# Kernel tuning notes

Measured on AMD Instinct MI355X. Metric: run time of the kernel, lower is better.

## Reference

```python
import jax, jax.numpy as jnp
import numpy as np

B, N, DIM, NL, E = 8, 4096, 128, 3, 524288
NN = B * N


def setup_inputs() -> dict:
    key = jax.random.key(0)
    kx, ke, kw = jax.random.split(key, 3)
    x = jax.random.normal(kx, (B, N, DIM), dtype=jnp.float32)
    batch_edge_index = jax.random.randint(ke, (2, E), 0, NN, dtype=jnp.int32)
    wks = jax.random.split(kw, NL)
    Ws = jnp.stack([jax.random.normal(k, (DIM, DIM), dtype=jnp.float32) / np.sqrt(DIM)
                    for k in wks])  # [NL, DIM, DIM]
    bs = jnp.zeros((NL, DIM), dtype=jnp.float32)
    return {"x": x, "batch_edge_index": batch_edge_index, "Ws": Ws, "bs": bs}


def _gcn_layer(x, W, b, row, col, deg_inv_sqrt, n):
    # PyG GCNConv: h = x @ W; symmetric normalization over edges+self-loops;
    # scatter-add messages at targets (col); add bias.
    h = x @ W  # [n, DIM]
    norm = deg_inv_sqrt[row] * deg_inv_sqrt[col]  # [E+n]
    msg = h[row] * norm[:, None]  # gather at sources, scale
    return jax.ops.segment_sum(msg, col, num_segments=n) + b


def reference(x, batch_edge_index, Ws, bs):
    nb, npts, d = x.shape
    n = nb * npts
    h = x.reshape(n, d)
    # add self-loops once (same edge structure for all layers)
    loops = jnp.arange(n, dtype=batch_edge_index.dtype)
    row = jnp.concatenate([batch_edge_index[0], loops])
    col = jnp.concatenate([batch_edge_index[1], loops])
    deg = jax.ops.segment_sum(jnp.ones_like(col, dtype=h.dtype), col, num_segments=n)
    deg_inv_sqrt = jnp.where(deg > 0, jax.lax.rsqrt(jnp.maximum(deg, 1e-12)), 0.0)
    for i in range(NL):
        out = _gcn_layer(h, Ws[i], bs[i], row, col, deg_inv_sqrt, n)
        h = jax.nn.relu(h + out)  # residual + relu (dropout = identity in eval)
    return h.reshape(nb, npts, d)
```

## Files before the change

kernel.cpp:

```cpp
#include <hip/hip_runtime.h>


typedef __attribute__((ext_vector_type(8))) short short8;
typedef __attribute__((ext_vector_type(4))) float f32x4;
typedef __attribute__((ext_vector_type(2))) float f32x2;

__device__ inline ushort f2bf(float f) {
    union { float f; unsigned u; } v; v.f = f;
    unsigned u = v.u;
    return (ushort)((u + 0x7fffu + ((u >> 16) & 1u)) >> 16);
}
__device__ inline float2 bf2f(unsigned u) {
    union { unsigned i; float f; } a, b;
    a.i = u << 16;
    b.i = u & 0xffff0000u;
    return make_float2(a.f, b.f);
}

__global__ void k_deg(const int* __restrict__ col, int* __restrict__ deg, int E) {
    int i = blockIdx.x * blockDim.x + threadIdx.x;
    if (i < E) atomicAdd(&deg[col[i]], 1);
}

__global__ __launch_bounds__(256) void k_scan1(const int* __restrict__ deg,
                                               int* __restrict__ offs,
                                               int* __restrict__ bsum, int n) {
    __shared__ int sm[256];
    int t = threadIdx.x, i = blockIdx.x * 256 + t;
    int v = (i < n) ? deg[i] : 0;
    sm[t] = v;
    __syncthreads();
    for (int off = 1; off < 256; off <<= 1) {
        int u = (t >= off) ? sm[t - off] : 0;
        __syncthreads();
        sm[t] += u;
        __syncthreads();
    }
    if (i < n) offs[i] = sm[t] - v;
    if (t == 255) bsum[blockIdx.x] = sm[255];
}

__global__ __launch_bounds__(128) void k_scan2(int* __restrict__ bsum, int nb) {
    __shared__ int sm[128];
    int t = threadIdx.x;
    int v = (t < nb) ? bsum[t] : 0;
    sm[t] = v;
    __syncthreads();
    for (int off = 1; off < 128; off <<= 1) {
        int u = (t >= off) ? sm[t - off] : 0;
        __syncthreads();
        sm[t] += u;
        __syncthreads();
    }
    if (t < nb) bsum[t] = sm[t] - v;
}

__global__ __launch_bounds__(256) void k_scan3(int* __restrict__ offs,
                                               const int* __restrict__ bsum,
                                               const int* __restrict__ deg,
                                               int* __restrict__ cnt,
                                               float* __restrict__ dis,
                                               int n, int E) {
    int i = blockIdx.x * 256 + threadIdx.x;
    if (i < n) {
        int o = offs[i] + bsum[blockIdx.x];
        offs[i] = o;
        cnt[i] = o;
        dis[i] = rsqrtf((float)(deg[i] + 1));
    }
    if (i == 0) offs[n] = E;
}

__global__ void k_csr(const int* __restrict__ row, const int* __restrict__ col,
                      int* __restrict__ cnt, ushort* __restrict__ csru, int E) {
    int i = blockIdx.x * blockDim.x + threadIdx.x;
    if (i < E) {
        int c = col[i];
        int p = atomicAdd(&cnt[c], 1);
        csru[p] = (ushort)row[i];
    }
}

__global__ void k_cvt(const float* __restrict__ x, unsigned* __restrict__ hb,
                      unsigned* __restrict__ g, int n) {
    int i = blockIdx.x * blockDim.x + threadIdx.x;
    if (i < n * 64) {
        float2 v = ((const float2*)x)[i];
        hb[i] = ((unsigned)f2bf(v.y) << 16) | f2bf(v.x);
    }
    if (i < 64) g[(size_t)n * 64 + i] = 0;
}

__global__ __launch_bounds__(256) void k_gemm(const unsigned* __restrict__ hb,
                                              const float* __restrict__ W,
                                              const float* __restrict__ dis,
                                              ushort* __restrict__ g, int n) {
    __shared__ unsigned Wl[128][64];
    int tid = threadIdx.x;
    {
        int nn = tid & 127, hf = tid >> 7;
        for (int q = 0; q < 32; ++q) {
            int k2 = hf * 32 + q;
            float lo = W[(size_t)(2 * k2) * 128 + nn];
            float hi = W[(size_t)(2 * k2 + 1) * 128 + nn];
            Wl[nn][k2 ^ ((nn & 7) << 2)] = ((unsigned)f2bf(hi) << 16) | f2bf(lo);
        }
    }
    __syncthreads();

    int w = tid >> 6, l = tid & 63;
    int rb = blockIdx.x * 64 + w * 16;
    int c = l & 15, q = l >> 4;

    const short8* arow = (const short8*)(hb + (size_t)(rb + c) * 64);
    short8 a0 = arow[q], a1 = arow[4 + q], a2 = arow[8 + q], a3 = arow[12 + q];

    f32x4 acc[8] = {};
#pragma unroll
    for (int nf = 0; nf < 8; ++nf) {
        const unsigned* wr = &Wl[nf * 16 + c][0];
        int s = (c & 7) << 2;
        int b = q * 4;
        short8 b0 = *(const short8*)(wr + ((b +  0) ^ s));
        short8 b1 = *(const short8*)(wr + ((b + 16) ^ s));
        short8 b2 = *(const short8*)(wr + ((b + 32) ^ s));
        short8 b3 = *(const short8*)(wr + ((b + 48) ^ s));
        acc[nf] = __builtin_amdgcn_mfma_f32_16x16x32_bf16(a0, b0, acc[nf], 0, 0, 0);
        acc[nf] = __builtin_amdgcn_mfma_f32_16x16x32_bf16(a1, b1, acc[nf], 0, 0, 0);
        acc[nf] = __builtin_amdgcn_mfma_f32_16x16x32_bf16(a2, b2, acc[nf], 0, 0, 0);
        acc[nf] = __builtin_amdgcn_mfma_f32_16x16x32_bf16(a3, b3, acc[nf], 0, 0, 0);
    }

    float d0 = dis[rb + q * 4 + 0], d1 = dis[rb + q * 4 + 1];
    float d2 = dis[rb + q * 4 + 2], d3 = dis[rb + q * 4 + 3];
#pragma unroll
    for (int nf = 0; nf < 8; ++nf) {
        int gc = nf * 16 + c;
        g[(size_t)(rb + q * 4 + 0) * 128 + gc] = f2bf(acc[nf][0] * d0);
        g[(size_t)(rb + q * 4 + 1) * 128 + gc] = f2bf(acc[nf][1] * d1);
        g[(size_t)(rb + q * 4 + 2) * 128 + gc] = f2bf(acc[nf][2] * d2);
        g[(size_t)(rb + q * 4 + 3) * 128 + gc] = f2bf(acc[nf][3] * d3);
    }
}

__global__ __launch_bounds__(256) void k_gather(const unsigned* __restrict__ g,
                                                unsigned* __restrict__ hb,
                                                const float* __restrict__ dis,
                                                const float2* __restrict__ bias2,
                                                const int* __restrict__ offs,
                                                const ushort* __restrict__ csru,
                                                float* __restrict__ outp,
                                                int n, int last) {
    int wid = threadIdx.x >> 6, lane = threadIdx.x & 63;
    int node = blockIdx.x * 4 + wid;
    if (node >= n) return;
    size_t nb = (size_t)node * 64 + lane;
    float2 acc = bf2f(g[nb]);
    int s = offs[node];
    int deg = offs[node + 1] - s;
    for (int j0 = 0; j0 < deg; j0 += 64) {
        int rem = deg - j0;
        int m = rem < 64 ? rem : 64;
        int idx = (lane < m) ? (int)__builtin_nontemporal_load(&csru[s + j0 + lane]) : n;
        int mc = (m + 15) & ~15;
        for (int t = 0; t < mc; t += 16) {
            unsigned v[16];
#pragma unroll
            for (int u = 0; u < 16; ++u)
                v[u] = g[(size_t)__shfl(idx, t + u, 64) * 64 + lane];
            float2 p0, p1;
#define ACC2(A, B, O)  p0 = bf2f(v[A]); p1 = bf2f(v[B]); \
                       O.x = p0.x + p1.x; O.y = p0.y + p1.y;
            float2 s0, s1, s2, s3, s4, s5, s6, s7;
            ACC2(0, 1, s0)  ACC2(2, 3, s1)  ACC2(4, 5, s2)  ACC2(6, 7, s3)
            ACC2(8, 9, s4)  ACC2(10, 11, s5) ACC2(12, 13, s6) ACC2(14, 15, s7)
#undef ACC2
            s0.x += s1.x; s2.x += s3.x; s4.x += s5.x; s6.x += s7.x;
            s0.y += s1.y; s2.y += s3.y; s4.y += s5.y; s6.y += s7.y;
            acc.x += (s0.x + s2.x) + (s4.x + s6.x);
            acc.y += (s0.y + s2.y) + (s4.y + s6.y);
        }
    }
    float d = dis[node];
    float2 bv = bias2[lane];
    float2 hv = bf2f(hb[nb]);
    float ox = fmaxf(hv.x + acc.x * d + bv.x, 0.f);
    float oy = fmaxf(hv.y + acc.y * d + bv.y, 0.f);
    if (last) {
        f32x2 o = { ox, oy };
        __builtin_nontemporal_store(o, (f32x2*)&outp[(size_t)node * 128 + lane * 2]);
    } else {
        hb[nb] = ((unsigned)f2bf(oy) << 16) | f2bf(ox);
    }
}

static inline size_t al256(size_t x) { return (x + 255) & ~(size_t)255; }

extern "C" void kernel_launch(void* const* d_in, const int* in_sizes, int n_in,
                              void* d_out, int out_size, void* d_ws, size_t ws_size,
                              hipStream_t stream) {
    const float* x  = (const float*)d_in[0];
    const int*   ei = (const int*)d_in[1];
    const float* Ws = (const float*)d_in[2];
    const float* bs = (const float*)d_in[3];
    int n  = in_sizes[0] / 128;
    int E  = in_sizes[1] / 2;
    int NL = in_sizes[2] / (128 * 128);
    const int* rowp = ei;
    const int* colp = ei + E;

    char* ws = (char*)d_ws;
    size_t plane = al256((size_t)(n + 1) * 256);
    unsigned* g  = (unsigned*)ws;
    unsigned* hb = (unsigned*)(ws + plane);
    char* p = ws + 2 * plane;
    float* dis  = (float*)p;               p += al256((size_t)n * 4);
    int*   deg  = (int*)p;                 p += al256((size_t)n * 4);
    int*   offs = (int*)p;                 p += al256((size_t)(n + 1) * 4);
    int*   cnt  = (int*)p;                 p += al256((size_t)n * 4);
    int*   bsum = (int*)p;                 p += 512;
    ushort* csru = (ushort*)p;

    int nb = (n + 255) / 256;

    (void)hipMemsetAsync(deg, 0, (size_t)n * 4, stream);
    k_deg<<<(E + 255) / 256, 256, 0, stream>>>(colp, deg, E);
    k_scan1<<<nb, 256, 0, stream>>>(deg, offs, bsum, n);
    k_scan2<<<1, 128, 0, stream>>>(bsum, nb);
    k_scan3<<<nb, 256, 0, stream>>>(offs, bsum, deg, cnt, dis, n, E);
    k_csr<<<(E + 255) / 256, 256, 0, stream>>>(rowp, colp, cnt, csru, E);
    k_cvt<<<(n * 64 + 255) / 256, 256, 0, stream>>>(x, hb, g, n);

    for (int l = 0; l < NL; ++l) {
        int last = (l + 1 == NL);
        k_gemm<<<n / 64, 256, 0, stream>>>(hb, Ws + (size_t)l * 128 * 128,
                                           dis, (ushort*)g, n);
        k_gather<<<(n + 3) / 4, 256, 0, stream>>>(g, hb, dis,
                                                  (const float2*)(bs + (size_t)l * 128),
                                                  offs, csru, (float*)d_out, n, last);
    }
}
```

Before: 165.0 us.

## Fuse fp32 input conversion into first GEMM and widen gather to 8-byte half-wave loads

```diff
diff --git a/kernel.cpp b/kernel.cpp
--- a/kernel.cpp
+++ b/kernel.cpp
@@ -3,7 +3,6 @@
 
 typedef __attribute__((ext_vector_type(8))) short short8;
 typedef __attribute__((ext_vector_type(4))) float f32x4;
-typedef __attribute__((ext_vector_type(2))) float f32x2;
 
 __device__ inline ushort f2bf(float f) {
     union { float f; unsigned u; } v; v.f = f;
@@ -15,6 +14,16 @@
     a.i = u << 16;
     b.i = u & 0xffff0000u;
     return make_float2(a.f, b.f);
+}
+__device__ inline f32x4 bf4(uint2 v) {
+    float2 a = bf2f(v.x), b = bf2f(v.y);
+    f32x4 r = { a.x, a.y, b.x, b.y };
+    return r;
+}
+__device__ inline short8 pack8(f32x4 a, f32x4 b) {
+    short8 r = { (short)f2bf(a.x), (short)f2bf(a.y), (short)f2bf(a.z), (short)f2bf(a.w),
+                 (short)f2bf(b.x), (short)f2bf(b.y), (short)f2bf(b.z), (short)f2bf(b.w) };
+    return r;
 }
 
 __global__ void k_deg(const int* __restrict__ col, int* __restrict__ deg, int E) {
@@ -60,6 +69,7 @@
                                                const int* __restrict__ deg,
                                                int* __restrict__ cnt,
                                                float* __restrict__ dis,
+                                               unsigned* __restrict__ g,
                                                int n, int E) {
     int i = blockIdx.x * 256 + threadIdx.x;
     if (i < n) {
@@ -69,6 +79,7 @@
         dis[i] = rsqrtf((float)(deg[i] + 1));
     }
     if (i == 0) offs[n] = E;
+    if (i < 64) g[(size_t)n * 64 + i] = 0;
 }
 
 __global__ void k_csr(const int* __restrict__ row, const int* __restrict__ col,
@@ -81,81 +92,92 @@
     }
 }
 
-__global__ void k_cvt(const float* __restrict__ x, unsigned* __restrict__ hb,
-                      unsigned* __restrict__ g, int n) {
-    int i = blockIdx.x * blockDim.x + threadIdx.x;
-    if (i < n * 64) {
-        float2 v = ((const float2*)x)[i];
-        hb[i] = ((unsigned)f2bf(v.y) << 16) | f2bf(v.x);
-    }
-    if (i < 64) g[(size_t)n * 64 + i] = 0;
-}
+#define GEMM_BODY(A0, A1, A2, A3)                                               \
+    f32x4 acc[8] = {};                                                          \
+    _Pragma("unroll")                                                           \
+    for (int nf = 0; nf < 8; ++nf) {                                            \
+        const unsigned* wr = &Wl[nf * 16 + c][0];                               \
+        int sx = (c & 7) << 2;                                                  \
+        int b = q * 4;                                                          \
+        short8 b0 = *(const short8*)(wr + ((b +  0) ^ sx));                     \
+        short8 b1 = *(const short8*)(wr + ((b + 16) ^ sx));                     \
+        short8 b2 = *(const short8*)(wr + ((b + 32) ^ sx));                     \
+        short8 b3 = *(const short8*)(wr + ((b + 48) ^ sx));                     \
+        acc[nf] = __builtin_amdgcn_mfma_f32_16x16x32_bf16(A0, b0, acc[nf], 0, 0, 0); \
+        acc[nf] = __builtin_amdgcn_mfma_f32_16x16x32_bf16(A1, b1, acc[nf], 0, 0, 0); \
+        acc[nf] = __builtin_amdgcn_mfma_f32_16x16x32_bf16(A2, b2, acc[nf], 0, 0, 0); \
+        acc[nf] = __builtin_amdgcn_mfma_f32_16x16x32_bf16(A3, b3, acc[nf], 0, 0, 0); \
+    }                                                                           \
+    float d0 = dis[rb + q * 4 + 0], d1 = dis[rb + q * 4 + 1];                   \
+    float d2 = dis[rb + q * 4 + 2], d3 = dis[rb + q * 4 + 3];                   \
+    _Pragma("unroll")                                                           \
+    for (int nf = 0; nf < 8; ++nf) {                                            \
+        int gc = nf * 16 + c;                                                   \
+        g[(size_t)(rb + q * 4 + 0) * 128 + gc] = f2bf(acc[nf][0] * d0);         \
+        g[(size_t)(rb + q * 4 + 1) * 128 + gc] = f2bf(acc[nf][1] * d1);         \
+        g[(size_t)(rb + q * 4 + 2) * 128 + gc] = f2bf(acc[nf][2] * d2);         \
+        g[(size_t)(rb + q * 4 + 3) * 128 + gc] = f2bf(acc[nf][3] * d3);         \
+    }
+
+#define W_STAGE                                                                  \
+    __shared__ unsigned Wl[128][64];                                             \
+    int tid = threadIdx.x;                                                       \
+    {                                                                            \
+        int nn = tid & 127, hf = tid >> 7;                                       \
+        for (int qq = 0; qq < 32; ++qq) {                                        \
+            int k2 = hf * 32 + qq;                                               \
+            float lo = W[(size_t)(2 * k2) * 128 + nn];                           \
+            float hi = W[(size_t)(2 * k2 + 1) * 128 + nn];                       \
+            Wl[nn][k2 ^ ((nn & 7) << 2)] = ((unsigned)f2bf(hi) << 16) | f2bf(lo);\
+        }                                                                        \
+    }                                                                            \
+    __syncthreads();                                                             \
+    int w = tid >> 6, l = tid & 63;                                              \
+    int rb = blockIdx.x * 64 + w * 16;                                           \
+    int c = l & 15, q = l >> 4;
 
 __global__ __launch_bounds__(256) void k_gemm(const unsigned* __restrict__ hb,
                                               const float* __restrict__ W,
                                               const float* __restrict__ dis,
                                               ushort* __restrict__ g, int n) {
-    __shared__ unsigned Wl[128][64];
-    int tid = threadIdx.x;
-    {
-        int nn = tid & 127, hf = tid >> 7;
-        for (int q = 0; q < 32; ++q) {
-            int k2 = hf * 32 + q;
-            float lo = W[(size_t)(2 * k2) * 128 + nn];
-            float hi = W[(size_t)(2 * k2 + 1) * 128 + nn];
-            Wl[nn][k2 ^ ((nn & 7) << 2)] = ((unsigned)f2bf(hi) << 16) | f2bf(lo);
-        }
-    }
-    __syncthreads();
-
-    int w = tid >> 6, l = tid & 63;
-    int rb = blockIdx.x * 64 + w * 16;
-    int c = l & 15, q = l >> 4;
-
+    W_STAGE
     const short8* arow = (const short8*)(hb + (size_t)(rb + c) * 64);
     short8 a0 = arow[q], a1 = arow[4 + q], a2 = arow[8 + q], a3 = arow[12 + q];
-
-    f32x4 acc[8] = {};
-#pragma unroll
-    for (int nf = 0; nf < 8; ++nf) {
-        const unsigned* wr = &Wl[nf * 16 + c][0];
-        int s = (c & 7) << 2;
-        int b = q * 4;
-        short8 b0 = *(const short8*)(wr + ((b +  0) ^ s));
-        short8 b1 = *(const short8*)(wr + ((b + 16) ^ s));
-        short8 b2 = *(const short8*)(wr + ((b + 32) ^ s));
-        short8 b3 = *(const short8*)(wr + ((b + 48) ^ s));
-        acc[nf] = __builtin_amdgcn_mfma_f32_16x16x32_bf16(a0, b0, acc[nf], 0, 0, 0);
-        acc[nf] = __builtin_amdgcn_mfma_f32_16x16x32_bf16(a1, b1, acc[nf], 0, 0, 0);
-        acc[nf] = __builtin_amdgcn_mfma_f32_16x16x32_bf16(a2, b2, acc[nf], 0, 0, 0);
-        acc[nf] = __builtin_amdgcn_mfma_f32_16x16x32_bf16(a3, b3, acc[nf], 0, 0, 0);
-    }
-
-    float d0 = dis[rb + q * 4 + 0], d1 = dis[rb + q * 4 + 1];
-    float d2 = dis[rb + q * 4 + 2], d3 = dis[rb + q * 4 + 3];
-#pragma unroll
-    for (int nf = 0; nf < 8; ++nf) {
-        int gc = nf * 16 + c;
-        g[(size_t)(rb + q * 4 + 0) * 128 + gc] = f2bf(acc[nf][0] * d0);
-        g[(size_t)(rb + q * 4 + 1) * 128 + gc] = f2bf(acc[nf][1] * d1);
-        g[(size_t)(rb + q * 4 + 2) * 128 + gc] = f2bf(acc[nf][2] * d2);
-        g[(size_t)(rb + q * 4 + 3) * 128 + gc] = f2bf(acc[nf][3] * d3);
-    }
+    GEMM_BODY(a0, a1, a2, a3)
+}
+
+__global__ __launch_bounds__(256) void k_gemm0(const float* __restrict__ x,
+                                               const float* __restrict__ W,
+                                               const float* __restrict__ dis,
+                                               ushort* __restrict__ g, int n) {
+    W_STAGE
+    const f32x4* xr = (const f32x4*)(x + (size_t)(rb + c) * 128);
+    short8 a0 = pack8(xr[q * 2 +  0], xr[q * 2 +  1]);
+    short8 a1 = pack8(xr[q * 2 +  8], xr[q * 2 +  9]);
+    short8 a2 = pack8(xr[q * 2 + 16], xr[q * 2 + 17]);
+    short8 a3 = pack8(xr[q * 2 + 24], xr[q * 2 + 25]);
+    GEMM_BODY(a0, a1, a2, a3)
 }
 
 __global__ __launch_bounds__(256) void k_gather(const unsigned* __restrict__ g,
                                                 unsigned* __restrict__ hb,
                                                 const float* __restrict__ dis,
-                                                const float2* __restrict__ bias2,
+                                                const float* __restrict__ bias,
                                                 const int* __restrict__ offs,
                                                 const ushort* __restrict__ csru,
+                                                const float* __restrict__ xres,
                                                 float* __restrict__ outp,
-                                                int n, int last) {
+                                                int n, int use_x, int last) {
     int wid = threadIdx.x >> 6, lane = threadIdx.x & 63;
     int node = blockIdx.x * 4 + wid;
     if (node >= n) return;
-    size_t nb = (size_t)node * 64 + lane;
-    float2 acc = bf2f(g[nb]);
+    int half = lane >> 5, fl = lane & 31;
+    int fo8 = fl * 8;
+    const char* gb = (const char*)g;
+
+    uint2 sv = *(const uint2*)(gb + ((size_t)(half ? n : node) << 8) + fo8);
+    f32x4 acc = bf4(sv);
+
     int s = offs[node];
     int deg = offs[node + 1] - s;
     for (int j0 = 0; j0 < deg; j0 += 64) {
@@ -164,33 +186,43 @@
         int idx = (lane < m) ? (int)__builtin_nontemporal_load(&csru[s + j0 + lane]) : n;
         int mc = (m + 15) & ~15;
         for (int t = 0; t < mc; t += 16) {
-            unsigned v[16];
+            uint2 v[8];
 #pragma unroll
-            for (int u = 0; u < 16; ++u)
-                v[u] = g[(size_t)__shfl(idx, t + u, 64) * 64 + lane];
-            float2 p0, p1;
-#define ACC2(A, B, O)  p0 = bf2f(v[A]); p1 = bf2f(v[B]); \
-                       O.x = p0.x + p1.x; O.y = p0.y + p1.y;
-            float2 s0, s1, s2, s3, s4, s5, s6, s7;
-            ACC2(0, 1, s0)  ACC2(2, 3, s1)  ACC2(4, 5, s2)  ACC2(6, 7, s3)
-            ACC2(8, 9, s4)  ACC2(10, 11, s5) ACC2(12, 13, s6) ACC2(14, 15, s7)
-#undef ACC2
-            s0.x += s1.x; s2.x += s3.x; s4.x += s5.x; s6.x += s7.x;
-            s0.y += s1.y; s2.y += s3.y; s4.y += s5.y; s6.y += s7.y;
-            acc.x += (s0.x + s2.x) + (s4.x + s6.x);
-            acc.y += (s0.y + s2.y) + (s4.y + s6.y);
+            for (int u = 0; u < 8; ++u) {
+                int r = __shfl(idx, t + 2 * u + half, 64);
+                v[u] = *(const uint2*)(gb + ((size_t)r << 8) + fo8);
+            }
+            f32x4 s0 = (bf4(v[0]) + bf4(v[1])) + (bf4(v[2]) + bf4(v[3]));
+            f32x4 s1 = (bf4(v[4]) + bf4(v[5])) + (bf4(v[6]) + bf4(v[7]));
+            acc += s0 + s1;
         }
     }
-    float d = dis[node];
-    float2 bv = bias2[lane];
-    float2 hv = bf2f(hb[nb]);
-    float ox = fmaxf(hv.x + acc.x * d + bv.x, 0.f);
-    float oy = fmaxf(hv.y + acc.y * d + bv.y, 0.f);
-    if (last) {
-        f32x2 o = { ox, oy };
-        __builtin_nontemporal_store(o, (f32x2*)&outp[(size_t)node * 128 + lane * 2]);
-    } else {
-        hb[nb] = ((unsigned)f2bf(oy) << 16) | f2bf(ox);
+    acc.x += __shfl_xor(acc.x, 32, 64);
+    acc.y += __shfl_xor(acc.y, 32, 64);
+    acc.z += __shfl_xor(acc.z, 32, 64);
+    acc.w += __shfl_xor(acc.w, 32, 64);
+
+    if (half == 0) {
+        float d = dis[node];
+        f32x4 bv = ((const f32x4*)bias)[fl];
+        f32x4 hv;
+        if (use_x) {
+            hv = ((const f32x4*)xres)[(size_t)node * 32 + fl];
+        } else {
+            uint2 h2 = *(const uint2*)((const char*)hb + ((size_t)node << 8) + fo8);
+            hv = bf4(h2);
+        }
+        f32x4 o = acc * d + hv + bv;
+        o.x = fmaxf(o.x, 0.f); o.y = fmaxf(o.y, 0.f);
+        o.z = fmaxf(o.z, 0.f); o.w = fmaxf(o.w, 0.f);
+        if (last) {
+            __builtin_nontemporal_store(o, (f32x4*)&outp[(size_t)node * 128 + fl * 4]);
+        } else {
+            uint2 pk;
+            pk.x = ((unsigned)f2bf(o.y) << 16) | f2bf(o.x);
+            pk.y = ((unsigned)f2bf(o.w) << 16) | f2bf(o.z);
+            *(uint2*)((char*)hb + ((size_t)node << 8) + fo8) = pk;
+        }
     }
 }
 
@@ -227,16 +259,20 @@
     k_deg<<<(E + 255) / 256, 256, 0, stream>>>(colp, deg, E);
     k_scan1<<<nb, 256, 0, stream>>>(deg, offs, bsum, n);
     k_scan2<<<1, 128, 0, stream>>>(bsum, nb);
-    k_scan3<<<nb, 256, 0, stream>>>(offs, bsum, deg, cnt, dis, n, E);
+    k_scan3<<<nb, 256, 0, stream>>>(offs, bsum, deg, cnt, dis, g, n, E);
     k_csr<<<(E + 255) / 256, 256, 0, stream>>>(rowp, colp, cnt, csru, E);
-    k_cvt<<<(n * 64 + 255) / 256, 256, 0, stream>>>(x, hb, g, n);
 
     for (int l = 0; l < NL; ++l) {
         int last = (l + 1 == NL);
-        k_gemm<<<n / 64, 256, 0, stream>>>(hb, Ws + (size_t)l * 128 * 128,
-                                           dis, (ushort*)g, n);
+        const float* Wl = Ws + (size_t)l * 128 * 128;
+        if (l == 0)
+            k_gemm0<<<n / 64, 256, 0, stream>>>(x, Wl, dis, (ushort*)g, n);
+        else
+            k_gemm<<<n / 64, 256, 0, stream>>>(hb, Wl, dis, (ushort*)g, n);
         k_gather<<<(n + 3) / 4, 256, 0, stream>>>(g, hb, dis,
-                                                  (const float2*)(bs + (size_t)l * 128),
-                                                  offs, csru, (float*)d_out, n, last);
-    }
-}
+                                                  bs + (size_t)l * 128,
+                                                  offs, csru, x,
+                                                  (float*)d_out, n,
+                                                  l == 0, last);
+    }
+}
```

New measurement: 168.7 us. 1.02x slower.
